# Performance work log

Hardware: AMD Instinct MI355X
Metric: run time of the kernel (lower is better)

## Reference

```python
import jax, jax.numpy as jnp
import numpy as np

N_NODES = 50000
N_EDGES = 800000
IN_DIM = 128
OUT_DIM = 64
LEAKY_SLOPE = 0.01  # torch F.leaky_relu default


def setup_inputs() -> dict:
    key = jax.random.key(0)
    k1, k2, k3, k4, k5 = jax.random.split(key, 5)
    features = jax.random.normal(k1, (N_NODES, IN_DIM), dtype=jnp.float32)
    src = jax.random.randint(k2, (N_EDGES,), 0, N_NODES, dtype=jnp.int32)
    dst = jax.random.randint(k3, (N_EDGES,), 0, N_NODES, dtype=jnp.int32)
    # fc: Linear(in_dim, out_dim, bias=False) -> stored as [in_dim, out_dim]
    W_fc = jax.random.normal(k4, (IN_DIM, OUT_DIM), dtype=jnp.float32) * (1.0 / np.sqrt(IN_DIM))
    # attn_fc: Linear(2*out_dim, 1, bias=False) -> stored as flat [2*out_dim]
    a_vec = jax.random.normal(k5, (2 * OUT_DIM,), dtype=jnp.float32) * (1.0 / np.sqrt(2 * OUT_DIM))
    return {"features": features, "src": src, "dst": dst, "W_fc": W_fc, "a_vec": a_vec}


def reference(features, src, dst, W_fc, a_vec):
    n = features.shape[0]
    d = W_fc.shape[1]
    # node projection: z = fc(features)
    z = features @ W_fc                                   # [N, d]
    # attn score: a^T [z_src || z_dst] = (z @ a_src)[src] + (z @ a_dst)[dst]
    az_src = z @ a_vec[:d]                                # [N]
    az_dst = z @ a_vec[d:]                                # [N]
    e = jax.nn.leaky_relu(az_src[src] + az_dst[dst], negative_slope=LEAKY_SLOPE)  # [E]
    # segment softmax over edges grouped by destination node
    e_max = jax.ops.segment_max(e, dst, num_segments=n)   # [N] (-inf for isolated nodes)
    e_exp = jnp.exp(e - e_max[dst])                       # [E]
    e_sum = jax.ops.segment_sum(e_exp, dst, num_segments=n)  # [N]
    alpha = e_exp / e_sum[dst]                            # [E]
    # weighted scatter-sum of source features to destination nodes
    h = jax.ops.segment_sum(alpha[:, None] * z[src], dst, num_segments=n)  # [N, d]
    return h
```

## Files before the change

### kernel.cpp

```cpp
#include <hip/hip_runtime.h>
#include <hip/hip_bf16.h>
#include <math.h>

#define N_NODES 50000
#define N_EDGES 800000
#define IN_DIM  128
#define OUT_DIM 64
#define LEAKY   0.01f

#define PROJ_ROWS 64
#define PROJ_NB   ((N_NODES + PROJ_ROWS - 1) / PROJ_ROWS)

#define SCAN_B   1024
#define SCAN_NB  ((N_NODES + SCAN_B - 1) / SCAN_B)

__global__ __launch_bounds__(256) void proj_kernel(
        const float* __restrict__ feat, const float* __restrict__ W,
        const float* __restrict__ a,
        __hip_bfloat16* __restrict__ zb,
        float* __restrict__ az_src, float* __restrict__ az_dst) {
    __shared__ float fs[PROJ_ROWS * IN_DIM];
    int tid  = threadIdx.x;
    int row0 = blockIdx.x * PROJ_ROWS;
    int nrows = N_NODES - row0; if (nrows > PROJ_ROWS) nrows = PROJ_ROWS;

    const float4* gsrc = (const float4*)(feat + (size_t)row0 * IN_DIM);
    if (nrows == PROJ_ROWS) {
#pragma unroll
        for (int i = 0; i < 8; ++i) {
            int idx = tid + i * 256;
            ((float4*)fs)[idx] = gsrc[idx];
        }
    } else {
        int lim = nrows * (IN_DIM / 4);
#pragma unroll
        for (int i = 0; i < 8; ++i) {
            int idx = tid + i * 256;
            if (idx < lim) ((float4*)fs)[idx] = gsrc[idx];
        }
    }
    __syncthreads();

    int lane  = tid & 63;
    int rbase = (tid >> 6) * 16;

    float acc[16];
#pragma unroll
    for (int r = 0; r < 16; ++r) acc[r] = 0.f;

    for (int kk = 0; kk < IN_DIM / 4; ++kk) {
        float w0 = W[(kk * 4 + 0) * OUT_DIM + lane];
        float w1 = W[(kk * 4 + 1) * OUT_DIM + lane];
        float w2 = W[(kk * 4 + 2) * OUT_DIM + lane];
        float w3 = W[(kk * 4 + 3) * OUT_DIM + lane];
#pragma unroll
        for (int r = 0; r < 16; ++r) {
            float4 f = *(const float4*)&fs[(rbase + r) * IN_DIM + kk * 4];
            acc[r] = fmaf(f.x, w0, acc[r]);
            acc[r] = fmaf(f.y, w1, acc[r]);
            acc[r] = fmaf(f.z, w2, acc[r]);
            acc[r] = fmaf(f.w, w3, acc[r]);
        }
    }

    float a1 = a[lane], a2 = a[OUT_DIM + lane];
#pragma unroll
    for (int r = 0; r < 16; ++r) {
        int row = row0 + rbase + r;
        if (row < N_NODES) {
            zb[(size_t)row * OUT_DIM + lane] = __float2bfloat16(acc[r]);
            float s1 = acc[r] * a1;
            float s2 = acc[r] * a2;
#pragma unroll
            for (int off = 32; off > 0; off >>= 1) {
                s1 += __shfl_xor(s1, off, 64);
                s2 += __shfl_xor(s2, off, 64);
            }
            if (lane == r) { az_src[row] = s1; az_dst[row] = s2; }
        }
    }
}

__global__ __launch_bounds__(256) void hist_kernel(
        const int* __restrict__ dst, int* __restrict__ counts,
        int* __restrict__ rank) {
    int i = blockIdx.x * 256 + threadIdx.x;
    if (i < N_EDGES) rank[i] = atomicAdd(&counts[dst[i]], 1);
}

__global__ __launch_bounds__(SCAN_B) void scan1_kernel(
        const int* __restrict__ counts, int* __restrict__ offsets,
        int* __restrict__ blocksums) {
    __shared__ int s[SCAN_B];
    int i = blockIdx.x * SCAN_B + threadIdx.x;
    int v = (i < N_NODES) ? counts[i] : 0;
    s[threadIdx.x] = v;
    __syncthreads();
    for (int off = 1; off < SCAN_B; off <<= 1) {
        int t = (threadIdx.x >= off) ? s[threadIdx.x - off] : 0;
        __syncthreads();
        s[threadIdx.x] += t;
        __syncthreads();
    }
    if (i < N_NODES) offsets[i] = s[threadIdx.x] - v;
    if (threadIdx.x == SCAN_B - 1) blocksums[blockIdx.x] = s[SCAN_B - 1];
}

__global__ __launch_bounds__(SCAN_B) void scan3_kernel(
        int* __restrict__ offsets, const int* __restrict__ blocksums) {
    __shared__ int bs[64];
    if (threadIdx.x < 64) {
        int lane = threadIdx.x;
        int v = (lane < SCAN_NB) ? blocksums[lane] : 0;
        int inc = v;
#pragma unroll
        for (int off = 1; off < 64; off <<= 1) {
            int t = __shfl_up(inc, off, 64);
            if (lane >= off) inc += t;
        }
        bs[lane] = inc - v;
    }
    __syncthreads();
    int i = blockIdx.x * SCAN_B + threadIdx.x;
    if (i < N_NODES) offsets[i] += bs[blockIdx.x];
    if (i == 0) offsets[N_NODES] = N_EDGES;
}

__global__ __launch_bounds__(256) void build_csr_kernel(
        const int* __restrict__ src, const int* __restrict__ dst,
        const int* __restrict__ rank, const int* __restrict__ offsets,
        int* __restrict__ src_sorted) {
    int i = blockIdx.x * 256 + threadIdx.x;
    if (i >= N_EDGES) return;
    int t = dst[i];
    int pos = offsets[t] + rank[i];
    src_sorted[pos] = src[i];
}

__global__ __launch_bounds__(256) void node_fused_kernel(
        const int* __restrict__ offsets, const int* __restrict__ src_sorted,
        const float* __restrict__ az_src, const float* __restrict__ az_dst,
        const __hip_bfloat16* __restrict__ zb, float* __restrict__ h) {
    int lane = threadIdx.x & 63;
    int w    = threadIdx.x >> 6;
    int t    = blockIdx.x * 4 + w;
    if (t >= N_NODES) return;
    int beg = offsets[t];
    int end = offsets[t + 1];
    float az_d = az_dst[t];

    float acc0 = 0.f, acc1 = 0.f, acc2 = 0.f, acc3 = 0.f;
    float ss0 = 0.f, ss1 = 0.f, ss2 = 0.f, ss3 = 0.f;
    int i = beg;
    for (; i + 4 <= end; i += 4) {
        int s0 = src_sorted[i];
        int s1 = src_sorted[i + 1];
        int s2 = src_sorted[i + 2];
        int s3 = src_sorted[i + 3];
        float v0 = az_src[s0] + az_d;
        float v1 = az_src[s1] + az_d;
        float v2 = az_src[s2] + az_d;
        float v3 = az_src[s3] + az_d;
        v0 = v0 > 0.f ? v0 : LEAKY * v0;
        v1 = v1 > 0.f ? v1 : LEAKY * v1;
        v2 = v2 > 0.f ? v2 : LEAKY * v2;
        v3 = v3 > 0.f ? v3 : LEAKY * v3;
        float x0 = __expf(v0), x1 = __expf(v1);
        float x2 = __expf(v2), x3 = __expf(v3);
        ss0 += x0; ss1 += x1; ss2 += x2; ss3 += x3;
        acc0 = fmaf(x0, __bfloat162float(zb[(size_t)s0 * OUT_DIM + lane]), acc0);
        acc1 = fmaf(x1, __bfloat162float(zb[(size_t)s1 * OUT_DIM + lane]), acc1);
        acc2 = fmaf(x2, __bfloat162float(zb[(size_t)s2 * OUT_DIM + lane]), acc2);
        acc3 = fmaf(x3, __bfloat162float(zb[(size_t)s3 * OUT_DIM + lane]), acc3);
    }
    for (; i < end; ++i) {
        int s0 = src_sorted[i];
        float v0 = az_src[s0] + az_d;
        v0 = v0 > 0.f ? v0 : LEAKY * v0;
        float x0 = __expf(v0);
        ss0 += x0;
        acc0 = fmaf(x0, __bfloat162float(zb[(size_t)s0 * OUT_DIM + lane]), acc0);
    }
    float ssum = (ss0 + ss1) + (ss2 + ss3);
    float inv  = (end > beg) ? 1.f / ssum : 0.f;
    h[(size_t)t * OUT_DIM + lane] = ((acc0 + acc1) + (acc2 + acc3)) * inv;
}

extern "C" void kernel_launch(void* const* d_in, const int* in_sizes, int n_in,
                              void* d_out, int out_size, void* d_ws, size_t ws_size,
                              hipStream_t stream) {
    const float* feat = (const float*)d_in[0];
    const int*   src  = (const int*)  d_in[1];
    const int*   dst  = (const int*)  d_in[2];
    const float* W    = (const float*)d_in[3];
    const float* a    = (const float*)d_in[4];
    float* h = (float*)d_out;

    float* az_src     = (float*)d_ws;
    float* az_dst     = az_src + N_NODES;
    int*   counts     = (int*)(az_dst + N_NODES);
    int*   offsets    = counts + N_NODES;
    int*   blocksums  = offsets + N_NODES + 1;
    int*   rank       = blocksums + 64;
    int*   src_sorted = rank + N_EDGES;
    __hip_bfloat16* zb = (__hip_bfloat16*)(src_sorted + N_EDGES);

    hipMemsetAsync(counts, 0, sizeof(int) * N_NODES, stream);

    int eblocks = (N_EDGES + 255) / 256;
    hist_kernel<<<eblocks, 256, 0, stream>>>(dst, counts, rank);
    scan1_kernel<<<SCAN_NB, SCAN_B, 0, stream>>>(counts, offsets, blocksums);
    scan3_kernel<<<SCAN_NB, SCAN_B, 0, stream>>>(offsets, blocksums);

    proj_kernel<<<PROJ_NB, 256, 0, stream>>>(feat, W, a, zb, az_src, az_dst);

    build_csr_kernel<<<eblocks, 256, 0, stream>>>(src, dst, rank, offsets,
                                                  src_sorted);

    node_fused_kernel<<<(N_NODES + 3) / 4, 256, 0, stream>>>(
        offsets, src_sorted, az_src, az_dst, zb, h);
}
```

Before: 202.1 us.

## Merge scans into single-block scan, halve projection rows, nontemporal CSR stores

Replaces the two-kernel block scan with one single-block kernel in which each thread serially sums and then writes a contiguous chunk of counts, removing one launch and the blocksums buffer. Halves PROJ_ROWS to 32, which doubles the number of projection blocks and lowers per-thread register use. Uses nontemporal stores for the scattered src_sorted writes in the CSR build. The single-block scan runs on one CU with strided per-thread reads, which may be slower than the multi-block version, and the smaller projection tile reloads W more often.

```diff
diff --git a/kernel.cpp b/kernel.cpp
--- a/kernel.cpp
+++ b/kernel.cpp
@@ -8,11 +8,12 @@
 #define OUT_DIM 64
 #define LEAKY   0.01f
 
-#define PROJ_ROWS 64
+#define PROJ_ROWS 32
 #define PROJ_NB   ((N_NODES + PROJ_ROWS - 1) / PROJ_ROWS)
-
-#define SCAN_B   1024
-#define SCAN_NB  ((N_NODES + SCAN_B - 1) / SCAN_B)
+#define EDGE_NB   ((N_EDGES + 255) / 256)
+
+#define SCAN_T   1024
+#define PER_T    ((N_NODES + SCAN_T) / SCAN_T + 1)
 
 __global__ __launch_bounds__(256) void proj_kernel(
         const float* __restrict__ feat, const float* __restrict__ W,
@@ -27,14 +28,14 @@
     const float4* gsrc = (const float4*)(feat + (size_t)row0 * IN_DIM);
     if (nrows == PROJ_ROWS) {
 #pragma unroll
-        for (int i = 0; i < 8; ++i) {
+        for (int i = 0; i < 4; ++i) {
             int idx = tid + i * 256;
             ((float4*)fs)[idx] = gsrc[idx];
         }
     } else {
         int lim = nrows * (IN_DIM / 4);
 #pragma unroll
-        for (int i = 0; i < 8; ++i) {
+        for (int i = 0; i < 4; ++i) {
             int idx = tid + i * 256;
             if (idx < lim) ((float4*)fs)[idx] = gsrc[idx];
         }
@@ -42,11 +43,11 @@
     __syncthreads();
 
     int lane  = tid & 63;
-    int rbase = (tid >> 6) * 16;
-
-    float acc[16];
-#pragma unroll
-    for (int r = 0; r < 16; ++r) acc[r] = 0.f;
+    int rbase = (tid >> 6) * 8;
+
+    float acc[8];
+#pragma unroll
+    for (int r = 0; r < 8; ++r) acc[r] = 0.f;
 
     for (int kk = 0; kk < IN_DIM / 4; ++kk) {
         float w0 = W[(kk * 4 + 0) * OUT_DIM + lane];
@@ -54,7 +55,7 @@
         float w2 = W[(kk * 4 + 2) * OUT_DIM + lane];
         float w3 = W[(kk * 4 + 3) * OUT_DIM + lane];
 #pragma unroll
-        for (int r = 0; r < 16; ++r) {
+        for (int r = 0; r < 8; ++r) {
             float4 f = *(const float4*)&fs[(rbase + r) * IN_DIM + kk * 4];
             acc[r] = fmaf(f.x, w0, acc[r]);
             acc[r] = fmaf(f.y, w1, acc[r]);
@@ -65,7 +66,7 @@
 
     float a1 = a[lane], a2 = a[OUT_DIM + lane];
 #pragma unroll
-    for (int r = 0; r < 16; ++r) {
+    for (int r = 0; r < 8; ++r) {
         int row = row0 + rbase + r;
         if (row < N_NODES) {
             zb[(size_t)row * OUT_DIM + lane] = __float2bfloat16(acc[r]);
@@ -88,42 +89,33 @@
     if (i < N_EDGES) rank[i] = atomicAdd(&counts[dst[i]], 1);
 }
 
-__global__ __launch_bounds__(SCAN_B) void scan1_kernel(
-        const int* __restrict__ counts, int* __restrict__ offsets,
-        int* __restrict__ blocksums) {
-    __shared__ int s[SCAN_B];
-    int i = blockIdx.x * SCAN_B + threadIdx.x;
-    int v = (i < N_NODES) ? counts[i] : 0;
-    s[threadIdx.x] = v;
+__global__ __launch_bounds__(SCAN_T) void scan_kernel(
+        const int* __restrict__ counts, int* __restrict__ offsets) {
+    __shared__ int s[SCAN_T];
+    int t = threadIdx.x;
+    int base = t * PER_T;
+
+    int sum = 0;
+    for (int j = 0; j < PER_T; ++j) {
+        int idx = base + j;
+        if (idx < N_NODES) sum += counts[idx];
+    }
+    s[t] = sum;
     __syncthreads();
-    for (int off = 1; off < SCAN_B; off <<= 1) {
-        int t = (threadIdx.x >= off) ? s[threadIdx.x - off] : 0;
+    for (int off = 1; off < SCAN_T; off <<= 1) {
+        int x = (t >= off) ? s[t - off] : 0;
         __syncthreads();
-        s[threadIdx.x] += t;
+        s[t] += x;
         __syncthreads();
     }
-    if (i < N_NODES) offsets[i] = s[threadIdx.x] - v;
-    if (threadIdx.x == SCAN_B - 1) blocksums[blockIdx.x] = s[SCAN_B - 1];
-}
-
-__global__ __launch_bounds__(SCAN_B) void scan3_kernel(
-        int* __restrict__ offsets, const int* __restrict__ blocksums) {
-    __shared__ int bs[64];
-    if (threadIdx.x < 64) {
-        int lane = threadIdx.x;
-        int v = (lane < SCAN_NB) ? blocksums[lane] : 0;
-        int inc = v;
-#pragma unroll
-        for (int off = 1; off < 64; off <<= 1) {
-            int t = __shfl_up(inc, off, 64);
-            if (lane >= off) inc += t;
-        }
-        bs[lane] = inc - v;
-    }
-    __syncthreads();
-    int i = blockIdx.x * SCAN_B + threadIdx.x;
-    if (i < N_NODES) offsets[i] += bs[blockIdx.x];
-    if (i == 0) offsets[N_NODES] = N_EDGES;
+    int run = s[t] - sum;
+    for (int j = 0; j < PER_T; ++j) {
+        int idx = base + j;
+        if (idx <= N_NODES) {
+            offsets[idx] = run;
+            if (idx < N_NODES) run += counts[idx];
+        }
+    }
 }
 
 __global__ __launch_bounds__(256) void build_csr_kernel(
@@ -134,7 +126,7 @@
     if (i >= N_EDGES) return;
     int t = dst[i];
     int pos = offsets[t] + rank[i];
-    src_sorted[pos] = src[i];
+    __builtin_nontemporal_store(src[i], &src_sorted[pos]);
 }
 
 __global__ __launch_bounds__(256) void node_fused_kernel(
@@ -200,21 +192,18 @@
     float* az_dst     = az_src + N_NODES;
     int*   counts     = (int*)(az_dst + N_NODES);
     int*   offsets    = counts + N_NODES;
-    int*   blocksums  = offsets + N_NODES + 1;
-    int*   rank       = blocksums + 64;
+    int*   rank       = offsets + N_NODES + 1;
     int*   src_sorted = rank + N_EDGES;
     __hip_bfloat16* zb = (__hip_bfloat16*)(src_sorted + N_EDGES);
 
     hipMemsetAsync(counts, 0, sizeof(int) * N_NODES, stream);
 
-    int eblocks = (N_EDGES + 255) / 256;
-    hist_kernel<<<eblocks, 256, 0, stream>>>(dst, counts, rank);
-    scan1_kernel<<<SCAN_NB, SCAN_B, 0, stream>>>(counts, offsets, blocksums);
-    scan3_kernel<<<SCAN_NB, SCAN_B, 0, stream>>>(offsets, blocksums);
+    hist_kernel<<<EDGE_NB, 256, 0, stream>>>(dst, counts, rank);
+    scan_kernel<<<1, SCAN_T, 0, stream>>>(counts, offsets);
 
     proj_kernel<<<PROJ_NB, 256, 0, stream>>>(feat, W, a, zb, az_src, az_dst);
 
-    build_csr_kernel<<<eblocks, 256, 0, stream>>>(src, dst, rank, offsets,
+    build_csr_kernel<<<EDGE_NB, 256, 0, stream>>>(src, dst, rank, offsets,
                                                   src_sorted);
 
     node_fused_kernel<<<(N_NODES + 3) / 4, 256, 0, stream>>>(
```

Measured after the change: 292.4 us. 44.7% more time.
